# Optimization experiments

Hardware: AMD Instinct MI355X
Metric: run time of the kernel (lower is better)

Reference implementation:

```python
import jax, jax.numpy as jnp
import numpy as np


def setup_inputs() -> dict:
    key = jax.random.key(0)
    k1, k2 = jax.random.split(key)
    x = jax.random.normal(k1, (32, 256, 128, 128), dtype=jnp.float32)
    conv_w = jax.random.normal(k2, (1, 2, 3, 3), dtype=jnp.float32) * 0.1
    return {"x": x, "conv_w": conv_w}


def reference(x, conv_w):
    # channel-wise mean and max -> [B,1,H,W] each
    avg_out = jnp.mean(x, axis=1, keepdims=True)
    max_out = jnp.max(x, axis=1, keepdims=True)
    cat = jnp.concatenate([avg_out, max_out], axis=1)  # [B,2,H,W]
    # 3x3 conv, 2->1 channels, padding=1, no bias (NCHW, OIHW)
    y = jax.lax.conv_general_dilated(
        cat, conv_w,
        window_strides=(1, 1),
        padding=((1, 1), (1, 1)),
        dimension_numbers=("NCHW", "OIHW", "NCHW"),
    )  # [B,1,H,W]
    # note: original returns conv_out * sigmoid(conv_out) (SiLU of conv output)
    return y * jax.nn.sigmoid(y)
```

## Files before the change

kernel.cpp:

```cpp
#include <hip/hip_runtime.h>

#define BATCH 32
#define CH    256
#define HH    128
#define WW    128
#define HW    (HH * WW)
#define HW4   (HW / 4)

__global__ __launch_bounds__(256) void reduce_mean_max(
    const float* __restrict__ x, float* __restrict__ red) {
    int idx = blockIdx.x * blockDim.x + threadIdx.x;
    int b  = idx >> 12;
    int p4 = idx & (HW4 - 1);

    const float4* xp = reinterpret_cast<const float4*>(x)
                       + (size_t)b * (size_t)CH * HW4 + p4;

    float4 v = xp[0];
    float4 s = v;
    float4 m = v;
    #pragma unroll 8
    for (int c = 1; c < CH; ++c) {
        float4 t = xp[(size_t)c * HW4];
        s.x += t.x; s.y += t.y; s.z += t.z; s.w += t.w;
        m.x = fmaxf(m.x, t.x);
        m.y = fmaxf(m.y, t.y);
        m.z = fmaxf(m.z, t.z);
        m.w = fmaxf(m.w, t.w);
    }

    const float inv = 1.0f / (float)CH;
    float4 avg = make_float4(s.x * inv, s.y * inv, s.z * inv, s.w * inv);

    float4* rp = reinterpret_cast<float4*>(red) + (size_t)b * (2 * HW4) + p4;
    rp[0]   = avg;
    rp[HW4] = m;
}

__global__ __launch_bounds__(256) void conv3x3_silu(
    const float* __restrict__ red, const float* __restrict__ cw,
    float* __restrict__ out) {
    int idx = blockIdx.x * blockDim.x + threadIdx.x;
    int b  = idx >> 14;
    int hw = idx & (HW - 1);
    int h  = hw >> 7;
    int w  = hw & (WW - 1);

    float wreg[18];
    #pragma unroll
    for (int i = 0; i < 18; ++i) wreg[i] = cw[i];

    const float* base = red + (size_t)b * (2 * HW);
    float acc = 0.0f;
    #pragma unroll
    for (int ic = 0; ic < 2; ++ic) {
        #pragma unroll
        for (int kh = 0; kh < 3; ++kh) {
            int ih = h + kh - 1;
            if (ih < 0 || ih >= HH) continue;
            #pragma unroll
            for (int kw = 0; kw < 3; ++kw) {
                int iw = w + kw - 1;
                if (iw < 0 || iw >= WW) continue;
                acc += base[ic * HW + ih * WW + iw] * wreg[ic * 9 + kh * 3 + kw];
            }
        }
    }
    out[idx] = acc / (1.0f + expf(-acc));
}

extern "C" void kernel_launch(void* const* d_in, const int* in_sizes, int n_in,
                              void* d_out, int out_size, void* d_ws, size_t ws_size,
                              hipStream_t stream) {
    const float* x  = (const float*)d_in[0];
    const float* cw = (const float*)d_in[1];
    float* out = (float*)d_out;
    float* red = (float*)d_ws;

    reduce_mean_max<<<(BATCH * HW4) / 256, 256, 0, stream>>>(x, red);
    conv3x3_silu<<<(BATCH * HW) / 256, 256, 0, stream>>>(red, cw, out);
}
```

Baseline: 100.7 us.

## Tile conv through LDS with 4-wide outputs and use nontemporal loads in reduction

The reduction kernel now reads with nontemporal vector loads, unrolls deeper and starts from zero/-inf initial values. The conv kernel stages an 8-row halo tile of both reduced channels in shared memory, and each thread computes four adjacent outputs with a single float4 store. This cuts redundant global reads and per-pixel boundary branches in the conv. The reduction streams 1 GB of input and dominates total time, so the conv changes touch only a small share of it.

```diff
diff --git a/kernel.cpp b/kernel.cpp
--- a/kernel.cpp
+++ b/kernel.cpp
@@ -7,22 +7,23 @@
 #define HW    (HH * WW)
 #define HW4   (HW / 4)
 
+typedef float f32x4 __attribute__((ext_vector_type(4)));
+
 __global__ __launch_bounds__(256) void reduce_mean_max(
     const float* __restrict__ x, float* __restrict__ red) {
     int idx = blockIdx.x * blockDim.x + threadIdx.x;
     int b  = idx >> 12;
     int p4 = idx & (HW4 - 1);
 
-    const float4* xp = reinterpret_cast<const float4*>(x)
-                       + (size_t)b * (size_t)CH * HW4 + p4;
+    const f32x4* xp = reinterpret_cast<const f32x4*>(x)
+                      + (size_t)b * (size_t)CH * HW4 + p4;
 
-    float4 v = xp[0];
-    float4 s = v;
-    float4 m = v;
-    #pragma unroll 8
-    for (int c = 1; c < CH; ++c) {
-        float4 t = xp[(size_t)c * HW4];
-        s.x += t.x; s.y += t.y; s.z += t.z; s.w += t.w;
+    f32x4 s = {0.f, 0.f, 0.f, 0.f};
+    f32x4 m = {-INFINITY, -INFINITY, -INFINITY, -INFINITY};
+    #pragma unroll 16
+    for (int c = 0; c < CH; ++c) {
+        f32x4 t = __builtin_nontemporal_load(xp + (size_t)c * HW4);
+        s += t;
         m.x = fmaxf(m.x, t.x);
         m.y = fmaxf(m.y, t.y);
         m.z = fmaxf(m.z, t.z);
@@ -30,43 +31,78 @@
     }
 
     const float inv = 1.0f / (float)CH;
-    float4 avg = make_float4(s.x * inv, s.y * inv, s.z * inv, s.w * inv);
+    f32x4 avg = s * inv;
 
-    float4* rp = reinterpret_cast<float4*>(red) + (size_t)b * (2 * HW4) + p4;
+    f32x4* rp = reinterpret_cast<f32x4*>(red) + (size_t)b * (2 * HW4) + p4;
     rp[0]   = avg;
     rp[HW4] = m;
 }
 
+#define TROWS 8
+#define LW    (WW + 2)
+
 __global__ __launch_bounds__(256) void conv3x3_silu(
     const float* __restrict__ red, const float* __restrict__ cw,
     float* __restrict__ out) {
-    int idx = blockIdx.x * blockDim.x + threadIdx.x;
-    int b  = idx >> 14;
-    int hw = idx & (HW - 1);
-    int h  = hw >> 7;
-    int w  = hw & (WW - 1);
+    __shared__ float lin[2][TROWS + 2][LW];
 
-    float wreg[18];
+    int blk = blockIdx.x;
+    int b   = blk >> 4;
+    int r0  = (blk & 15) * TROWS;
+    int tid = threadIdx.x;
+
+    if (tid < 2 * (TROWS + 2)) {
+        int ch  = tid / (TROWS + 2);
+        int row = tid - ch * (TROWS + 2);
+        lin[ch][row][0]      = 0.f;
+        lin[ch][row][LW - 1] = 0.f;
+    }
+
+    const float4* red4 = reinterpret_cast<const float4*>(red);
+    for (int l = tid; l < 640; l += 256) {
+        int ch  = l / 320;
+        int rem = l - ch * 320;
+        int row = rem >> 5;
+        int c4  = rem & 31;
+        int gr  = r0 - 1 + row;
+        float4 v = make_float4(0.f, 0.f, 0.f, 0.f);
+        if (gr >= 0 && gr < HH)
+            v = red4[((size_t)b * 2 + ch) * HW4 + gr * 32 + c4];
+        float* dst = &lin[ch][row][1 + 4 * c4];
+        dst[0] = v.x; dst[1] = v.y; dst[2] = v.z; dst[3] = v.w;
+    }
+
+    float wg[18];
     #pragma unroll
-    for (int i = 0; i < 18; ++i) wreg[i] = cw[i];
+    for (int i = 0; i < 18; ++i) wg[i] = cw[i];
 
-    const float* base = red + (size_t)b * (2 * HW);
-    float acc = 0.0f;
+    __syncthreads();
+
+    int lr = tid >> 5;
+    int w0 = (tid & 31) * 4;
+
+    float acc[4] = {0.f, 0.f, 0.f, 0.f};
     #pragma unroll
-    for (int ic = 0; ic < 2; ++ic) {
+    for (int ch = 0; ch < 2; ++ch) {
         #pragma unroll
-        for (int kh = 0; kh < 3; ++kh) {
-            int ih = h + kh - 1;
-            if (ih < 0 || ih >= HH) continue;
+        for (int dr = 0; dr < 3; ++dr) {
+            const float* rowp = &lin[ch][lr + dr][w0];
+            float e[6];
             #pragma unroll
-            for (int kw = 0; kw < 3; ++kw) {
-                int iw = w + kw - 1;
-                if (iw < 0 || iw >= WW) continue;
-                acc += base[ic * HW + ih * WW + iw] * wreg[ic * 9 + kh * 3 + kw];
-            }
+            for (int k = 0; k < 6; ++k) e[k] = rowp[k];
+            const float* wp = &wg[ch * 9 + dr * 3];
+            #pragma unroll
+            for (int j = 0; j < 4; ++j)
+                acc[j] += e[j] * wp[0] + e[j + 1] * wp[1] + e[j + 2] * wp[2];
         }
     }
-    out[idx] = acc / (1.0f + expf(-acc));
+
+    float4 o;
+    o.x = acc[0] / (1.f + expf(-acc[0]));
+    o.y = acc[1] / (1.f + expf(-acc[1]));
+    o.z = acc[2] / (1.f + expf(-acc[2]));
+    o.w = acc[3] / (1.f + expf(-acc[3]));
+    reinterpret_cast<float4*>(out)[(size_t)b * HW4 + (r0 + lr) * 32 + (w0 >> 2)] = o;
 }
 
 extern "C" void kernel_launch(void* const* d_in, const int* in_sizes, int n_in,
@@ -78,5 +114,5 @@
     float* red = (float*)d_ws;
 
     reduce_mean_max<<<(BATCH * HW4) / 256, 256, 0, stream>>>(x, red);
-    conv3x3_silu<<<(BATCH * HW) / 256, 256, 0, stream>>>(red, cw, out);
+    conv3x3_silu<<<BATCH * (HH / TROWS), 256, 0, stream>>>(red, cw, out);
 }
```

After: 94.29 us, median of 2. 1.07x faster.
